# Optimization experiments

Hardware: AMD Instinct MI355X
Metric: run time of the kernel (lower is better)

Reference implementation:

```python
import jax, jax.numpy as jnp
import numpy as np

B, S, D, H, DH = 2, 2048, 1024, 16, 64

def setup_inputs() -> dict:
    key = jax.random.key(0)
    ks = jax.random.split(key, 9)
    sc = 0.02
    return {
        "x":  jax.random.normal(ks[0], (B, S, D), jnp.float32),
        "Wq": jax.random.normal(ks[1], (H, D, DH), jnp.float32) * sc,
        "bq": jax.random.normal(ks[2], (H, DH), jnp.float32) * sc,
        "Wk": jax.random.normal(ks[3], (H, D, DH), jnp.float32) * sc,
        "bk": jax.random.normal(ks[4], (H, DH), jnp.float32) * sc,
        "Wv": jax.random.normal(ks[5], (H, D, DH), jnp.float32) * sc,
        "bv": jax.random.normal(ks[6], (H, DH), jnp.float32) * sc,
        "Wo": jax.random.normal(ks[7], (D, D), jnp.float32) * sc,
        "bo": jax.random.normal(ks[8], (D,), jnp.float32) * sc,
    }

def reference(x, Wq, bq, Wk, bk, Wv, bv, Wo, bo):
    # Fused version of the per-head Python loop: all H heads batched.
    # q,k,v: [B,H,S,DH]
    q = jnp.einsum("bsi,hid->bhsd", x, Wq) + bq[None, :, None, :]
    k = jnp.einsum("bsi,hid->bhsd", x, Wk) + bk[None, :, None, :]
    v = jnp.einsum("bsi,hid->bhsd", x, Wv) + bv[None, :, None, :]
    scale = 1.0 / jnp.sqrt(jnp.asarray(DH, x.dtype))
    scores = jnp.einsum("bhsd,bhtd->bhst", q, k) * scale  # [B,H,S,S]
    attn = jax.nn.softmax(scores, axis=-1)
    o = jnp.einsum("bhst,bhtd->bhsd", attn, v)            # [B,H,S,DH]
    # torch.cat([head_0,...,head_{H-1}], dim=-1) -> [B,S,H*DH]
    o = jnp.transpose(o, (0, 2, 1, 3)).reshape(B, S, H * DH)
    # Dropout is identity in eval mode; final dense projection.
    return jnp.einsum("bsi,io->bso", o, Wo) + bo
```

## Files before the change

### kernel.cpp

```cpp
#include <hip/hip_runtime.h>
#include <hip/hip_bf16.h>

#define BB 2
#define SS 2048
#define DD 1024
#define HH 16
#define DHH 64

typedef __attribute__((ext_vector_type(8))) __bf16 bf16x8;
typedef __attribute__((ext_vector_type(4))) float f32x4;
typedef __attribute__((ext_vector_type(16))) float f32x16;
typedef __attribute__((ext_vector_type(4))) int i32x4;
typedef __attribute__((ext_vector_type(4))) unsigned int u32x4;

#define MFMA16 __builtin_amdgcn_mfma_f32_16x16x32_bf16
#define MFMA32 __builtin_amdgcn_mfma_f32_32x32x16_bf16

__device__ __forceinline__ unsigned short f2b(float f) {
  __hip_bfloat16 h = __float2bfloat16(f);
  unsigned short u;
  __builtin_memcpy(&u, &h, 2);
  return u;
}

__device__ __forceinline__ float exp2_fast(float x) {
  float r;
  asm("v_exp_f32 %0, %1" : "=v"(r) : "v"(x));
  return r;
}

__device__ __forceinline__ unsigned int cvtpk_bf16(float lo, float hi) {
  unsigned int r;
  asm("v_cvt_pk_bf16_f32 %0, %1, %2" : "=v"(r) : "v"(lo), "v"(hi));
  return r;
}

__device__ __forceinline__ void gl_lds16(const void* g, void* l) {
  __builtin_amdgcn_global_load_lds((const __attribute__((address_space(1))) void*)g,
                                   (__attribute__((address_space(3))) void*)l, 16, 0, 0);
}

__global__ __launch_bounds__(256) void k_cast(const float* __restrict__ in,
                                              unsigned short* __restrict__ out, int n4) {
  int i = blockIdx.x * blockDim.x + threadIdx.x;
  if (i >= n4) return;
  float4 v = ((const float4*)in)[i];
  ushort4 o;
  o.x = f2b(v.x); o.y = f2b(v.y); o.z = f2b(v.z); o.w = f2b(v.w);
  ((ushort4*)out)[i] = o;
}

__global__ __launch_bounds__(256) void k_tcast(const float* __restrict__ in,
                                               unsigned short* __restrict__ out, int R, int C) {
  __shared__ float t[32][33];
  size_t mb = (size_t)blockIdx.z * R * C;
  const float* im = in + mb;
  unsigned short* om = out + mb;
  int c0 = blockIdx.x * 32, r0 = blockIdx.y * 32;
  int tx = threadIdx.x & 31, ty = threadIdx.x >> 5;
#pragma unroll
  for (int rr = ty; rr < 32; rr += 8)
    t[rr][tx] = im[(size_t)(r0 + rr) * C + c0 + tx];
  __syncthreads();
#pragma unroll
  for (int rr = ty; rr < 32; rr += 8)
    om[(size_t)(c0 + rr) * R + r0 + tx] = f2b(t[tx][rr]);
}

__global__ __launch_bounds__(256) void k_tcast3(const float* __restrict__ Wq,
                                                const float* __restrict__ Wk,
                                                const float* __restrict__ Wv,
                                                unsigned short* __restrict__ out) {
  __shared__ float t[32][33];
  int z = blockIdx.z;
  const float* im = (z < 16 ? Wq : (z < 32 ? Wk : Wv)) + (size_t)(z & 15) * DD * DHH;
  unsigned short* om = out + (size_t)z * DD * DHH;
  int c0 = blockIdx.x * 32, r0 = blockIdx.y * 32;
  int tx = threadIdx.x & 31, ty = threadIdx.x >> 5;
#pragma unroll
  for (int rr = ty; rr < 32; rr += 8)
    t[rr][tx] = im[(size_t)(r0 + rr) * DHH + c0 + tx];
  __syncthreads();
#pragma unroll
  for (int rr = ty; rr < 32; rr += 8)
    om[(size_t)(c0 + rr) * DD + r0 + tx] = f2b(t[tx][rr]);
}

__global__ __launch_bounds__(256) void k_qkv(const unsigned short* __restrict__ A,
                                             const unsigned short* __restrict__ Wt,
                                             const float* __restrict__ bq,
                                             const float* __restrict__ bk,
                                             const float* __restrict__ bv,
                                             unsigned short* __restrict__ Qb,
                                             unsigned short* __restrict__ Kb,
                                             unsigned short* __restrict__ Vtb) {
  __shared__ __align__(16) unsigned short As[128 * 64];
  __shared__ __align__(16) unsigned short Bs[128 * 64];
  int tid = threadIdx.x;
  int w = tid >> 6, l = tid & 63, lr = l & 15, lg = l >> 4;
  int wr = w >> 1, wc = w & 1;
  int col0 = blockIdx.x * 128, row0 = blockIdx.y * 128;
  int sel = col0 >> 10;
  bool vsel = (sel == 2);
  const float* biasp = sel == 0 ? bq : (sel == 1 ? bk : bv);
  unsigned short* outp = sel == 0 ? Qb : Kb;
  float qscale = sel == 0 ? 0.18033688011112042f : 1.0f;

  int r8 = l >> 3, c8 = l & 7;
  const unsigned short* Ab = A + (size_t)(row0 + w * 32 + r8) * DD + c8 * 8;
  const unsigned short* Bb = Wt + (size_t)(col0 + w * 32 + r8) * DD + c8 * 8;

  f32x4 zero = {0.f, 0.f, 0.f, 0.f};
  f32x4 acc[4][4];
#pragma unroll
  for (int m = 0; m < 4; m++)
#pragma unroll
    for (int n = 0; n < 4; n++) acc[m][n] = zero;

  for (int k0 = 0; k0 < DD; k0 += 64) {
    __syncthreads();
#pragma unroll
    for (int c = 0; c < 4; c++) {
      gl_lds16(Ab + (size_t)c * 8 * DD + k0, (char*)As + (w * 32 + c * 8) * 128);
      gl_lds16(Bb + (size_t)c * 8 * DD + k0, (char*)Bs + (w * 32 + c * 8) * 128);
    }
    __syncthreads();
#pragma unroll
    for (int kk = 0; kk < 2; kk++) {
      bf16x8 af[4], bfr[4];
#pragma unroll
      for (int m = 0; m < 4; m++)
        af[m] = *(const bf16x8*)&As[(wr * 64 + m * 16 + lr) * 64 + kk * 32 + lg * 8];
#pragma unroll
      for (int n = 0; n < 4; n++)
        bfr[n] = *(const bf16x8*)&Bs[(wc * 64 + n * 16 + lr) * 64 + kk * 32 + lg * 8];
      if (!vsel) {
#pragma unroll
        for (int m = 0; m < 4; m++)
#pragma unroll
          for (int n = 0; n < 4; n++)
            acc[m][n] = MFMA16(af[m], bfr[n], acc[m][n], 0, 0, 0);
      } else {
#pragma unroll
        for (int m = 0; m < 4; m++)
#pragma unroll
          for (int n = 0; n < 4; n++)
            acc[m][n] = MFMA16(bfr[n], af[m], acc[m][n], 0, 0, 0);
      }
    }
  }

  if (!vsel) {
#pragma unroll
    for (int n = 0; n < 4; n++) {
      int c = col0 + wc * 64 + n * 16 + lr;
      int h = (c >> 6) & 15;
      int d = c & 63;
      float bias = biasp[h * DHH + d];
#pragma unroll
      for (int m = 0; m < 4; m++) {
#pragma unroll
        for (int j = 0; j < 4; j++) {
          int row = row0 + wr * 64 + m * 16 + lg * 4 + j;
          int b = row >> 11, s = row & 2047;
          outp[((size_t)(b * HH + h) * SS + s) * DHH + d] = f2b((acc[m][n][j] + bias) * qscale);
        }
      }
    }
  } else {
    int b = row0 >> 11, s0 = row0 & 2047;
#pragma unroll
    for (int n = 0; n < 4; n++) {
#pragma unroll
      for (int j = 0; j < 4; j++) {
        int dl = wc * 64 + n * 16 + lg * 4 + j;
        int hh = ((col0 & 1023) + dl) >> 6;
        int d = dl & 63;
        float bias = bv[hh * DHH + d];
#pragma unroll
        for (int m = 0; m < 4; m++) {
          int sl = wr * 64 + m * 16 + lr;
          Vtb[((size_t)(b * HH + hh) * DHH + d) * SS + s0 + sl] = f2b(acc[m][n][j] + bias);
        }
      }
    }
  }
}

__global__ __launch_bounds__(256) void k_proj(const unsigned short* __restrict__ A,
                                              const unsigned short* __restrict__ Wt,
                                              const float* __restrict__ bo,
                                              float* __restrict__ out) {
  __shared__ __align__(16) unsigned short As[128 * 64];
  __shared__ __align__(16) unsigned short Bs[128 * 64];
  int tid = threadIdx.x;
  int w = tid >> 6, l = tid & 63, lr = l & 15, lg = l >> 4;
  int wr = w >> 1, wc = w & 1;
  int col0 = blockIdx.x * 128, row0 = blockIdx.y * 128;

  int r8 = l >> 3, c8 = l & 7;
  const unsigned short* Ab = A + (size_t)(row0 + w * 32 + r8) * DD + c8 * 8;
  const unsigned short* Bb = Wt + (size_t)(col0 + w * 32 + r8) * DD + c8 * 8;

  f32x4 zero = {0.f, 0.f, 0.f, 0.f};
  f32x4 acc[4][4];
#pragma unroll
  for (int m = 0; m < 4; m++)
#pragma unroll
    for (int n = 0; n < 4; n++) acc[m][n] = zero;

  for (int k0 = 0; k0 < DD; k0 += 64) {
    __syncthreads();
#pragma unroll
    for (int c = 0; c < 4; c++) {
      gl_lds16(Ab + (size_t)c * 8 * DD + k0, (char*)As + (w * 32 + c * 8) * 128);
      gl_lds16(Bb + (size_t)c * 8 * DD + k0, (char*)Bs + (w * 32 + c * 8) * 128);
    }
    __syncthreads();
#pragma unroll
    for (int kk = 0; kk < 2; kk++) {
      bf16x8 af[4], bfr[4];
#pragma unroll
      for (int m = 0; m < 4; m++)
        af[m] = *(const bf16x8*)&As[(wr * 64 + m * 16 + lr) * 64 + kk * 32 + lg * 8];
#pragma unroll
      for (int n = 0; n < 4; n++)
        bfr[n] = *(const bf16x8*)&Bs[(wc * 64 + n * 16 + lr) * 64 + kk * 32 + lg * 8];
#pragma unroll
      for (int m = 0; m < 4; m++)
#pragma unroll
        for (int n = 0; n < 4; n++)
          acc[m][n] = MFMA16(af[m], bfr[n], acc[m][n], 0, 0, 0);
    }
  }

#pragma unroll
  for (int n = 0; n < 4; n++) {
    int c = col0 + wc * 64 + n * 16 + lr;
    float bias = bo[c];
#pragma unroll
    for (int m = 0; m < 4; m++) {
#pragma unroll
      for (int j = 0; j < 4; j++) {
        int row = row0 + wr * 64 + m * 16 + lg * 4 + j;
        out[(size_t)row * DD + c] = acc[m][n][j] + bias;
      }
    }
  }
}

#define QT 128
#define KVB 128
#define NTILE (SS / KVB)

__global__ __launch_bounds__(256, 2) void k_attn(const unsigned short* __restrict__ Q,
                                                 const unsigned short* __restrict__ K,
                                                 const unsigned short* __restrict__ Vt,
                                                 unsigned short* __restrict__ Ocat) {
  __shared__ __align__(16) char sm[81920];

  int tid = threadIdx.x;
  int w = tid >> 6, lane = tid & 63;
  int q32 = lane & 31, hi = lane >> 5;
  bool lo = (hi == 0);

  int n = blockIdx.x;
  int bh = ((n & 7) << 2) | ((n >> 3) & 3);
  int q0 = (n >> 5) * QT;
  int bi = bh >> 4, h = bh & 15;
  const unsigned short* Qm = Q + (size_t)bh * SS * DHH;
  const unsigned short* Km = K + (size_t)bh * SS * DHH;
  const unsigned short* Vm = Vt + (size_t)bh * DHH * SS;

  int l8r = lane >> 3, l8c = lane & 7;
  int cgK = l8c ^ l8r;
  int l16r = lane >> 4, l16c = lane & 15;

#pragma unroll
  for (int c = 0; c < 4; c++) {
    int base = w * 32 + c * 8;
    gl_lds16(Qm + (size_t)(q0 + base + l8r) * DHH + cgK * 8, sm + base * 128);
    gl_lds16(Km + (size_t)(base + l8r) * DHH + cgK * 8, sm + 16384 + base * 128);
  }
#pragma unroll
  for (int c = 0; c < 4; c++) {
    int based = w * 16 + c * 4;
    int cgV = l16c ^ (c * 4 + l16r);
    gl_lds16(Vm + (size_t)(based + l16r) * SS + cgV * 8, sm + 49152 + based * 256);
  }
  __syncthreads();

  bf16x8 qf[4];
  {
    int r = w * 32 + q32;
    const char* qb = sm + r * 128;
    int sw = (r & 7) << 4;
#pragma unroll
    for (int ks = 0; ks < 4; ks++)
      qf[ks] = *(const bf16x8*)(qb + ((ks * 32 + hi * 16) ^ sw));
  }

  f32x16 oacc0 = {}, oacc1 = {};
  float m_ = -1e30f, l_ = 0.f;
  const int sw3 = (q32 & 7) << 4;
  const int sw4 = (q32 & 15) << 4;

#define MKPA(PB, u) do { \
    unsigned int x0 = cvtpk_bf16(PB[8*(u)+0], PB[8*(u)+1]); \
    unsigned int x1 = cvtpk_bf16(PB[8*(u)+2], PB[8*(u)+3]); \
    unsigned int y0 = cvtpk_bf16(PB[8*(u)+4], PB[8*(u)+5]); \
    unsigned int y1 = cvtpk_bf16(PB[8*(u)+6], PB[8*(u)+7]); \
    unsigned int sx0 = (unsigned int)__shfl_xor((int)x0, 32); \
    unsigned int sx1 = (unsigned int)__shfl_xor((int)x1, 32); \
    unsigned int sy0 = (unsigned int)__shfl_xor((int)y0, 32); \
    unsigned int sy1 = (unsigned int)__shfl_xor((int)y1, 32); \
    pa[0] = lo ? x0 : sy0; pa[1] = lo ? x1 : sy1; \
    pa[2] = lo ? sx0 : y0; pa[3] = lo ? sx1 : y1; \
  } while (0)

#define PVSTEP(s) do { \
    bf16x8 pf = *(bf16x8*)&pa; \
    bf16x8 vf0 = *(const bf16x8*)(Vc + (q32) * 256 + (((s) * 32 + hi * 16) ^ sw4)); \
    bf16x8 vf1 = *(const bf16x8*)(Vc + (32 + q32) * 256 + (((s) * 32 + hi * 16) ^ sw4)); \
    oacc0 = MFMA32(vf0, pf, oacc0, 0, 0, 0); \
    oacc1 = MFMA32(vf1, pf, oacc1, 0, 0, 0); \
  } while (0)

  for (int t = 0; t < NTILE; t++) {
    const char* Kc = sm + 16384 + (t & 1) * 16384;
    const char* Vc = sm + 49152 + (t & 1) * 16384;

    if (t + 1 < NTILE) {
      int kv0 = (t + 1) * KVB;
      char* kd = sm + 16384 + ((t + 1) & 1) * 16384;
      char* vd = sm + 49152 + ((t + 1) & 1) * 16384;
#pragma unroll
      for (int c = 0; c < 4; c++) {
        int base = w * 32 + c * 8;
        gl_lds16(Km + (size_t)(kv0 + base + l8r) * DHH + cgK * 8, kd + base * 128);
      }
#pragma unroll
      for (int c = 0; c < 4; c++) {
        int based = w * 16 + c * 4;
        int cgV = l16c ^ (c * 4 + l16r);
        gl_lds16(Vm + (size_t)(based + l16r) * SS + kv0 + cgV * 8, vd + based * 256);
      }
    }

    f32x16 p0 = {}, p1 = {}, p2 = {}, p3 = {};
    __builtin_amdgcn_s_setprio(1);
#pragma unroll
    for (int ks = 0; ks < 4; ks++) {
      int co = (ks * 32 + hi * 16) ^ sw3;
      bf16x8 k0 = *(const bf16x8*)(Kc + (q32) * 128 + co);
      bf16x8 k1 = *(const bf16x8*)(Kc + (32 + q32) * 128 + co);
      bf16x8 k2 = *(const bf16x8*)(Kc + (64 + q32) * 128 + co);
      bf16x8 k3 = *(const bf16x8*)(Kc + (96 + q32) * 128 + co);
      p0 = MFMA32(k0, qf[ks], p0, 0, 0, 0);
      p1 = MFMA32(k1, qf[ks], p1, 0, 0, 0);
      p2 = MFMA32(k2, qf[ks], p2, 0, 0, 0);
      p3 = MFMA32(k3, qf[ks], p3, 0, 0, 0);
    }
    __builtin_amdgcn_s_setprio(0);

    float t16[16];
#pragma unroll
    for (int r = 0; r < 16; r++)
      t16[r] = fmaxf(fmaxf(p0[r], p1[r]), fmaxf(p2[r], p3[r]));
#pragma unroll
    for (int r = 0; r < 8; r++) t16[r] = fmaxf(t16[r], t16[r + 8]);
#pragma unroll
    for (int r = 0; r < 4; r++) t16[r] = fmaxf(t16[r], t16[r + 4]);
    float tmax = fmaxf(fmaxf(t16[0], t16[1]), fmaxf(t16[2], t16[3]));
    tmax = fmaxf(tmax, __shfl_xor(tmax, 32));

    if (__any(tmax > m_ + 8.0f)) {
      float nm = fmaxf(m_, tmax);
      float al = exp2_fast(m_ - nm);
      m_ = nm; l_ *= al;
#pragma unroll
      for (int r = 0; r < 16; r++) { oacc0[r] *= al; oacc1[r] *= al; }
    }

#pragma unroll
    for (int r = 0; r < 16; r++) p0[r] = exp2_fast(p0[r] - m_);
#pragma unroll
    for (int r = 0; r < 16; r++) p1[r] = exp2_fast(p1[r] - m_);
#pragma unroll
    for (int r = 0; r < 16; r++) p2[r] = exp2_fast(p2[r] - m_);
#pragma unroll
    for (int r = 0; r < 16; r++) p3[r] = exp2_fast(p3[r] - m_);
    float s16[16];
#pragma unroll
    for (int r = 0; r < 16; r++) s16[r] = (p0[r] + p1[r]) + (p2[r] + p3[r]);
#pragma unroll
    for (int r = 0; r < 8; r++) s16[r] += s16[r + 8];
#pragma unroll
    for (int r = 0; r < 4; r++) s16[r] += s16[r + 4];
    float ssum = (s16[0] + s16[1]) + (s16[2] + s16[3]);
    ssum += __shfl_xor(ssum, 32);
    l_ += ssum;

    __builtin_amdgcn_s_setprio(1);
    u32x4 pa;
    MKPA(p0, 0); PVSTEP(0);
    MKPA(p0, 1); PVSTEP(1);
    MKPA(p1, 0); PVSTEP(2);
    MKPA(p1, 1); PVSTEP(3);
    MKPA(p2, 0); PVSTEP(4);
    MKPA(p2, 1); PVSTEP(5);
    MKPA(p3, 0); PVSTEP(6);
    MKPA(p3, 1); PVSTEP(7);
    __builtin_amdgcn_s_setprio(0);

    __syncthreads();
  }

  float inv = 1.0f / l_;
  unsigned short* Os = (unsigned short*)sm;
  int rowq = w * 32 + q32;
#pragma unroll
  for (int r = 0; r < 16; r++) {
    int d = (r & 3) + 8 * (r >> 2) + 4 * hi;
    Os[rowq * 72 + d] = f2b(oacc0[r] * inv);
    Os[rowq * 72 + 32 + d] = f2b(oacc1[r] * inv);
  }
  __syncthreads();
#pragma unroll
  for (int i = 0; i < 4; i++) {
    int ci = tid + i * 256;
    int r = ci >> 3, c = ci & 7;
    i32x4 v = *(const i32x4*)(Os + r * 72 + c * 8);
    *(i32x4*)(Ocat + ((size_t)(bi * SS + q0 + r)) * DD + h * DHH + c * 8) = v;
  }
}

extern "C" void kernel_launch(void* const* d_in, const int* in_sizes, int n_in,
                              void* d_out, int out_size, void* d_ws, size_t ws_size,
                              hipStream_t stream) {
  const float* x  = (const float*)d_in[0];
  const float* Wq = (const float*)d_in[1];
  const float* bq = (const float*)d_in[2];
  const float* Wk = (const float*)d_in[3];
  const float* bk = (const float*)d_in[4];
  const float* Wv = (const float*)d_in[5];
  const float* bv = (const float*)d_in[6];
  const float* Wo = (const float*)d_in[7];
  const float* bo = (const float*)d_in[8];
  float* out = (float*)d_out;

  char* ws = (char*)d_ws;
  unsigned short* xb    = (unsigned short*)(ws);
  unsigned short* wqkvt = (unsigned short*)(ws + (size_t)(8u  << 20));
  unsigned short* wot   = (unsigned short*)(ws + (size_t)(14u << 20));
  unsigned short* Qb    = (unsigned short*)(ws + (size_t)(16u << 20));
  unsigned short* Kb    = (unsigned short*)(ws + (size_t)(24u << 20));
  unsigned short* Vt    = (unsigned short*)(ws + (size_t)(32u << 20));
  unsigned short* Ocat  = (unsigned short*)(ws + (size_t)(40u << 20));

  k_cast<<<(BB * SS * DD / 4 + 255) / 256, 256, 0, stream>>>(x, xb, BB * SS * DD / 4);
  k_tcast3<<<dim3(DHH / 32, DD / 32, 48), 256, 0, stream>>>(Wq, Wk, Wv, wqkvt);
  k_tcast<<<dim3(DD / 32, DD / 32, 1), 256, 0, stream>>>(Wo, wot, DD, DD);
  k_qkv<<<dim3(3 * DD / 128, BB * SS / 128), 256, 0, stream>>>(xb, wqkvt, bq, bk, bv, Qb, Kb, Vt);
  k_attn<<<dim3((SS / QT) * BB * HH), 256, 0, stream>>>(Qb, Kb, Vt, Ocat);
  k_proj<<<dim3(DD / 128, BB * SS / 128), 256, 0, stream>>>(Ocat, wot, bo, out);
}
```

Before: 141.1 us.

## Fuse prep casts, stage QKV epilogue via LDS, rewrite attention as single-wave register-streamed

Merges the three cast/transpose kernels into a single k_prep launch to cut launch overhead. The QKV GEMM epilogue now writes its tile to shared memory and stores 16-byte rows, replacing scattered 2-byte global writes for Q, K and transposed V. The attention kernel becomes one 64-lane wave per 32-query block. It loads K and V fragments straight from global memory into registers, double-buffering K across 64-key steps instead of using LDS tiles. This drops LDS traffic and barriers but relies on L2/cache hits for K/V reuse across blocks and has much less data sharing per block.

```diff
diff --git a/kernel.cpp b/kernel.cpp
--- a/kernel.cpp
+++ b/kernel.cpp
@@ -29,9 +29,9 @@
   return r;
 }
 
-__device__ __forceinline__ unsigned int cvtpk_bf16(float lo, float hi) {
+__device__ __forceinline__ unsigned int cvtpk_bf16(float lo_, float hi_) {
   unsigned int r;
-  asm("v_cvt_pk_bf16_f32 %0, %1, %2" : "=v"(r) : "v"(lo), "v"(hi));
+  asm("v_cvt_pk_bf16_f32 %0, %1, %2" : "=v"(r) : "v"(lo_), "v"(hi_));
   return r;
 }
 
@@ -40,23 +40,40 @@
                                    (__attribute__((address_space(3))) void*)l, 16, 0, 0);
 }
 
-__global__ __launch_bounds__(256) void k_cast(const float* __restrict__ in,
-                                              unsigned short* __restrict__ out, int n4) {
-  int i = blockIdx.x * blockDim.x + threadIdx.x;
-  if (i >= n4) return;
-  float4 v = ((const float4*)in)[i];
-  ushort4 o;
-  o.x = f2b(v.x); o.y = f2b(v.y); o.z = f2b(v.z); o.w = f2b(v.w);
-  ((ushort4*)out)[i] = o;
-}
-
-__global__ __launch_bounds__(256) void k_tcast(const float* __restrict__ in,
-                                               unsigned short* __restrict__ out, int R, int C) {
+__global__ __launch_bounds__(256) void k_prep(const float* __restrict__ x,
+                                              const float* __restrict__ Wq,
+                                              const float* __restrict__ Wk,
+                                              const float* __restrict__ Wv,
+                                              const float* __restrict__ Wo,
+                                              unsigned short* __restrict__ xb,
+                                              unsigned short* __restrict__ wqkvt,
+                                              unsigned short* __restrict__ wot) {
+  int blk = blockIdx.x;
+  if (blk < 4096) {
+    int i = blk * 256 + threadIdx.x;
+    float4 v = ((const float4*)x)[i];
+    ushort4 o;
+    o.x = f2b(v.x); o.y = f2b(v.y); o.z = f2b(v.z); o.w = f2b(v.w);
+    ((ushort4*)xb)[i] = o;
+    return;
+  }
   __shared__ float t[32][33];
-  size_t mb = (size_t)blockIdx.z * R * C;
-  const float* im = in + mb;
-  unsigned short* om = out + mb;
-  int c0 = blockIdx.x * 32, r0 = blockIdx.y * 32;
+  const float* im;
+  unsigned short* om;
+  int R, C, c0, r0;
+  if (blk < 7168) {
+    int bi2 = blk - 4096;
+    int z = bi2 >> 6, rem = bi2 & 63;
+    im = (z < 16 ? Wq : (z < 32 ? Wk : Wv)) + (size_t)(z & 15) * DD * DHH;
+    om = wqkvt + (size_t)z * DD * DHH;
+    R = DD; C = DHH;
+    c0 = (rem & 1) * 32; r0 = (rem >> 1) * 32;
+  } else {
+    int bi2 = blk - 7168;
+    im = Wo; om = wot;
+    R = DD; C = DD;
+    c0 = (bi2 & 31) * 32; r0 = (bi2 >> 5) * 32;
+  }
   int tx = threadIdx.x & 31, ty = threadIdx.x >> 5;
 #pragma unroll
   for (int rr = ty; rr < 32; rr += 8)
@@ -65,25 +82,6 @@
 #pragma unroll
   for (int rr = ty; rr < 32; rr += 8)
     om[(size_t)(c0 + rr) * R + r0 + tx] = f2b(t[tx][rr]);
-}
-
-__global__ __launch_bounds__(256) void k_tcast3(const float* __restrict__ Wq,
-                                                const float* __restrict__ Wk,
-                                                const float* __restrict__ Wv,
-                                                unsigned short* __restrict__ out) {
-  __shared__ float t[32][33];
-  int z = blockIdx.z;
-  const float* im = (z < 16 ? Wq : (z < 32 ? Wk : Wv)) + (size_t)(z & 15) * DD * DHH;
-  unsigned short* om = out + (size_t)z * DD * DHH;
-  int c0 = blockIdx.x * 32, r0 = blockIdx.y * 32;
-  int tx = threadIdx.x & 31, ty = threadIdx.x >> 5;
-#pragma unroll
-  for (int rr = ty; rr < 32; rr += 8)
-    t[rr][tx] = im[(size_t)(r0 + rr) * DHH + c0 + tx];
-  __syncthreads();
-#pragma unroll
-  for (int rr = ty; rr < 32; rr += 8)
-    om[(size_t)(c0 + rr) * DD + r0 + tx] = f2b(t[tx][rr]);
 }
 
 __global__ __launch_bounds__(256) void k_qkv(const unsigned short* __restrict__ A,
@@ -94,8 +92,9 @@
                                              unsigned short* __restrict__ Qb,
                                              unsigned short* __restrict__ Kb,
                                              unsigned short* __restrict__ Vtb) {
-  __shared__ __align__(16) unsigned short As[128 * 64];
-  __shared__ __align__(16) unsigned short Bs[128 * 64];
+  __shared__ __align__(16) unsigned short SMEM[128 * 136];
+  unsigned short* As = SMEM;
+  unsigned short* Bs = SMEM + 128 * 64;
   int tid = threadIdx.x;
   int w = tid >> 6, l = tid & 63, lr = l & 15, lg = l >> 4;
   int wr = w >> 1, wc = w & 1;
@@ -150,39 +149,59 @@
     }
   }
 
+  __syncthreads();
+  unsigned short* Ts = SMEM;
   if (!vsel) {
 #pragma unroll
     for (int n = 0; n < 4; n++) {
-      int c = col0 + wc * 64 + n * 16 + lr;
-      int h = (c >> 6) & 15;
-      int d = c & 63;
-      float bias = biasp[h * DHH + d];
+      int cl = wc * 64 + n * 16 + lr;
+      float bias = biasp[(col0 + cl) & 1023];
 #pragma unroll
       for (int m = 0; m < 4; m++) {
 #pragma unroll
         for (int j = 0; j < 4; j++) {
-          int row = row0 + wr * 64 + m * 16 + lg * 4 + j;
-          int b = row >> 11, s = row & 2047;
-          outp[((size_t)(b * HH + h) * SS + s) * DHH + d] = f2b((acc[m][n][j] + bias) * qscale);
+          int sl = wr * 64 + m * 16 + lg * 4 + j;
+          Ts[sl * 136 + cl] = f2b((acc[m][n][j] + bias) * qscale);
         }
       }
     }
+    __syncthreads();
+    int trow = tid >> 4, tc = tid & 15;
+#pragma unroll
+    for (int pass = 0; pass < 8; pass++) {
+      int sl = pass * 16 + trow;
+      int c0l = tc * 8;
+      i32x4 v = *(const i32x4*)&Ts[sl * 136 + c0l];
+      int c = col0 + c0l;
+      int hh = (c >> 6) & 15, d = c & 63;
+      int row = row0 + sl;
+      int b = row >> 11, s = row & 2047;
+      *(i32x4*)(outp + ((size_t)(b * HH + hh) * SS + s) * DHH + d) = v;
+    }
   } else {
-    int b = row0 >> 11, s0 = row0 & 2047;
 #pragma unroll
     for (int n = 0; n < 4; n++) {
 #pragma unroll
       for (int j = 0; j < 4; j++) {
-        int dl = wc * 64 + n * 16 + lg * 4 + j;
-        int hh = ((col0 & 1023) + dl) >> 6;
-        int d = dl & 63;
-        float bias = bv[hh * DHH + d];
+        int cl = wc * 64 + n * 16 + lg * 4 + j;
+        float bias = bv[((col0 & 1023) + cl) & 1023];
 #pragma unroll
         for (int m = 0; m < 4; m++) {
           int sl = wr * 64 + m * 16 + lr;
-          Vtb[((size_t)(b * HH + hh) * DHH + d) * SS + s0 + sl] = f2b(acc[m][n][j] + bias);
+          Ts[cl * 136 + sl] = f2b(acc[m][n][j] + bias);
         }
       }
+    }
+    __syncthreads();
+    int trow = tid >> 4, tc = tid & 15;
+    int b = row0 >> 11, s0 = row0 & 2047;
+#pragma unroll
+    for (int pass = 0; pass < 8; pass++) {
+      int cl = pass * 16 + trow;
+      int s8 = tc * 8;
+      i32x4 v = *(const i32x4*)&Ts[cl * 136 + s8];
+      int cg = (col0 & 1023) + cl;
+      *(i32x4*)(Vtb + (size_t)(b * 1024 + cg) * SS + s0 + s8) = v;
     }
   }
 }
@@ -249,61 +268,34 @@
   }
 }
 
-#define QT 128
-#define KVB 128
-#define NTILE (SS / KVB)
-
-__global__ __launch_bounds__(256, 2) void k_attn(const unsigned short* __restrict__ Q,
-                                                 const unsigned short* __restrict__ K,
-                                                 const unsigned short* __restrict__ Vt,
-                                                 unsigned short* __restrict__ Ocat) {
-  __shared__ __align__(16) char sm[81920];
-
-  int tid = threadIdx.x;
-  int w = tid >> 6, lane = tid & 63;
+__global__ __launch_bounds__(64, 2) void k_attn(const unsigned short* __restrict__ Q,
+                                                const unsigned short* __restrict__ K,
+                                                const unsigned short* __restrict__ Vt,
+                                                unsigned short* __restrict__ Ocat) {
+  __shared__ __align__(16) unsigned short Os[32 * 72];
+
+  int lane = threadIdx.x;
   int q32 = lane & 31, hi = lane >> 5;
   bool lo = (hi == 0);
 
   int n = blockIdx.x;
-  int bh = ((n & 7) << 2) | ((n >> 3) & 3);
-  int q0 = (n >> 5) * QT;
+  int bh = ((n & 7) << 2) | ((n >> 9) & 3);
+  int q0 = ((n >> 3) & 63) * 32;
   int bi = bh >> 4, h = bh & 15;
   const unsigned short* Qm = Q + (size_t)bh * SS * DHH;
-  const unsigned short* Km = K + (size_t)bh * SS * DHH;
-  const unsigned short* Vm = Vt + (size_t)bh * DHH * SS;
-
-  int l8r = lane >> 3, l8c = lane & 7;
-  int cgK = l8c ^ l8r;
-  int l16r = lane >> 4, l16c = lane & 15;
-
-#pragma unroll
-  for (int c = 0; c < 4; c++) {
-    int base = w * 32 + c * 8;
-    gl_lds16(Qm + (size_t)(q0 + base + l8r) * DHH + cgK * 8, sm + base * 128);
-    gl_lds16(Km + (size_t)(base + l8r) * DHH + cgK * 8, sm + 16384 + base * 128);
-  }
-#pragma unroll
-  for (int c = 0; c < 4; c++) {
-    int based = w * 16 + c * 4;
-    int cgV = l16c ^ (c * 4 + l16r);
-    gl_lds16(Vm + (size_t)(based + l16r) * SS + cgV * 8, sm + 49152 + based * 256);
-  }
-  __syncthreads();
+  const unsigned short* kp = K + (size_t)bh * SS * DHH + q32 * DHH + hi * 8;
+  const unsigned short* vp = Vt + (size_t)bh * DHH * SS + (size_t)q32 * SS + hi * 8;
 
   bf16x8 qf[4];
   {
-    int r = w * 32 + q32;
-    const char* qb = sm + r * 128;
-    int sw = (r & 7) << 4;
+    const unsigned short* qrow = Qm + (size_t)(q0 + q32) * DHH + hi * 8;
 #pragma unroll
     for (int ks = 0; ks < 4; ks++)
-      qf[ks] = *(const bf16x8*)(qb + ((ks * 32 + hi * 16) ^ sw));
+      qf[ks] = *(const bf16x8*)(qrow + ks * 16);
   }
 
   f32x16 oacc0 = {}, oacc1 = {};
   float m_ = -1e30f, l_ = 0.f;
-  const int sw3 = (q32 & 7) << 4;
-  const int sw4 = (q32 & 15) << 4;
 
 #define MKPA(PB, u) do { \
     unsigned int x0 = cvtpk_bf16(PB[8*(u)+0], PB[8*(u)+1]); \
@@ -320,119 +312,100 @@
 
 #define PVSTEP(s) do { \
     bf16x8 pf = *(bf16x8*)&pa; \
-    bf16x8 vf0 = *(const bf16x8*)(Vc + (q32) * 256 + (((s) * 32 + hi * 16) ^ sw4)); \
-    bf16x8 vf1 = *(const bf16x8*)(Vc + (32 + q32) * 256 + (((s) * 32 + hi * 16) ^ sw4)); \
-    oacc0 = MFMA32(vf0, pf, oacc0, 0, 0, 0); \
-    oacc1 = MFMA32(vf1, pf, oacc1, 0, 0, 0); \
+    oacc0 = MFMA32(vf[(s)], pf, oacc0, 0, 0, 0); \
+    oacc1 = MFMA32(vf[4 + (s)], pf, oacc1, 0, 0, 0); \
   } while (0)
 
-  for (int t = 0; t < NTILE; t++) {
-    const char* Kc = sm + 16384 + (t & 1) * 16384;
-    const char* Vc = sm + 49152 + (t & 1) * 16384;
-
-    if (t + 1 < NTILE) {
-      int kv0 = (t + 1) * KVB;
-      char* kd = sm + 16384 + ((t + 1) & 1) * 16384;
-      char* vd = sm + 49152 + ((t + 1) & 1) * 16384;
-#pragma unroll
-      for (int c = 0; c < 4; c++) {
-        int base = w * 32 + c * 8;
-        gl_lds16(Km + (size_t)(kv0 + base + l8r) * DHH + cgK * 8, kd + base * 128);
-      }
-#pragma unroll
-      for (int c = 0; c < 4; c++) {
-        int based = w * 16 + c * 4;
-        int cgV = l16c ^ (c * 4 + l16r);
-        gl_lds16(Vm + (size_t)(based + l16r) * SS + kv0 + cgV * 8, vd + based * 256);
-      }
-    }
-
-    f32x16 p0 = {}, p1 = {}, p2 = {}, p3 = {};
-    __builtin_amdgcn_s_setprio(1);
-#pragma unroll
-    for (int ks = 0; ks < 4; ks++) {
-      int co = (ks * 32 + hi * 16) ^ sw3;
-      bf16x8 k0 = *(const bf16x8*)(Kc + (q32) * 128 + co);
-      bf16x8 k1 = *(const bf16x8*)(Kc + (32 + q32) * 128 + co);
-      bf16x8 k2 = *(const bf16x8*)(Kc + (64 + q32) * 128 + co);
-      bf16x8 k3 = *(const bf16x8*)(Kc + (96 + q32) * 128 + co);
-      p0 = MFMA32(k0, qf[ks], p0, 0, 0, 0);
-      p1 = MFMA32(k1, qf[ks], p1, 0, 0, 0);
-      p2 = MFMA32(k2, qf[ks], p2, 0, 0, 0);
-      p3 = MFMA32(k3, qf[ks], p3, 0, 0, 0);
-    }
-    __builtin_amdgcn_s_setprio(0);
-
-    float t16[16];
-#pragma unroll
-    for (int r = 0; r < 16; r++)
-      t16[r] = fmaxf(fmaxf(p0[r], p1[r]), fmaxf(p2[r], p3[r]));
-#pragma unroll
-    for (int r = 0; r < 8; r++) t16[r] = fmaxf(t16[r], t16[r + 8]);
-#pragma unroll
-    for (int r = 0; r < 4; r++) t16[r] = fmaxf(t16[r], t16[r + 4]);
-    float tmax = fmaxf(fmaxf(t16[0], t16[1]), fmaxf(t16[2], t16[3]));
-    tmax = fmaxf(tmax, __shfl_xor(tmax, 32));
-
-    if (__any(tmax > m_ + 8.0f)) {
-      float nm = fmaxf(m_, tmax);
-      float al = exp2_fast(m_ - nm);
-      m_ = nm; l_ *= al;
-#pragma unroll
-      for (int r = 0; r < 16; r++) { oacc0[r] *= al; oacc1[r] *= al; }
-    }
-
-#pragma unroll
-    for (int r = 0; r < 16; r++) p0[r] = exp2_fast(p0[r] - m_);
-#pragma unroll
-    for (int r = 0; r < 16; r++) p1[r] = exp2_fast(p1[r] - m_);
-#pragma unroll
-    for (int r = 0; r < 16; r++) p2[r] = exp2_fast(p2[r] - m_);
-#pragma unroll
-    for (int r = 0; r < 16; r++) p3[r] = exp2_fast(p3[r] - m_);
-    float s16[16];
-#pragma unroll
-    for (int r = 0; r < 16; r++) s16[r] = (p0[r] + p1[r]) + (p2[r] + p3[r]);
-#pragma unroll
-    for (int r = 0; r < 8; r++) s16[r] += s16[r + 8];
-#pragma unroll
-    for (int r = 0; r < 4; r++) s16[r] += s16[r + 4];
-    float ssum = (s16[0] + s16[1]) + (s16[2] + s16[3]);
-    ssum += __shfl_xor(ssum, 32);
-    l_ += ssum;
-
-    __builtin_amdgcn_s_setprio(1);
-    u32x4 pa;
-    MKPA(p0, 0); PVSTEP(0);
-    MKPA(p0, 1); PVSTEP(1);
-    MKPA(p1, 0); PVSTEP(2);
-    MKPA(p1, 1); PVSTEP(3);
-    MKPA(p2, 0); PVSTEP(4);
-    MKPA(p2, 1); PVSTEP(5);
-    MKPA(p3, 0); PVSTEP(6);
-    MKPA(p3, 1); PVSTEP(7);
-    __builtin_amdgcn_s_setprio(0);
-
-    __syncthreads();
-  }
-
+#define ATTN_BODY(CUR, NXT, T) do { \
+    int kv0 = (T) * 64; \
+    bf16x8 vf[8]; \
+    _Pragma("unroll") \
+    for (int db = 0; db < 2; db++) \
+      _Pragma("unroll") \
+      for (int s = 0; s < 4; s++) \
+        vf[db * 4 + s] = *(const bf16x8*)(vp + (size_t)db * 32 * SS + kv0 + s * 16); \
+    f32x16 p0 = {}, p1 = {}; \
+    _Pragma("unroll") \
+    for (int ks = 0; ks < 4; ks++) { \
+      p0 = MFMA32(CUR[ks], qf[ks], p0, 0, 0, 0); \
+      p1 = MFMA32(CUR[4 + ks], qf[ks], p1, 0, 0, 0); \
+    } \
+    if ((T) + 1 < 32) { \
+      const unsigned short* kn = kp + (size_t)((T) + 1) * 64 * DHH; \
+      _Pragma("unroll") \
+      for (int b2 = 0; b2 < 2; b2++) \
+        _Pragma("unroll") \
+        for (int ks = 0; ks < 4; ks++) \
+          NXT[b2 * 4 + ks] = *(const bf16x8*)(kn + b2 * 32 * DHH + ks * 16); \
+    } \
+    float t8[8]; \
+    _Pragma("unroll") \
+    for (int r = 0; r < 8; r++) \
+      t8[r] = fmaxf(fmaxf(p0[r], p0[r + 8]), fmaxf(p1[r], p1[r + 8])); \
+    _Pragma("unroll") \
+    for (int r = 0; r < 4; r++) t8[r] = fmaxf(t8[r], t8[r + 4]); \
+    float tmax = fmaxf(fmaxf(t8[0], t8[1]), fmaxf(t8[2], t8[3])); \
+    tmax = fmaxf(tmax, __shfl_xor(tmax, 32)); \
+    if (__any(tmax > m_ + 8.0f)) { \
+      float nm = fmaxf(m_, tmax); \
+      float al = exp2_fast(m_ - nm); \
+      m_ = nm; l_ *= al; \
+      _Pragma("unroll") \
+      for (int r = 0; r < 16; r++) { oacc0[r] *= al; oacc1[r] *= al; } \
+    } \
+    _Pragma("unroll") \
+    for (int r = 0; r < 16; r++) p0[r] = exp2_fast(p0[r] - m_); \
+    _Pragma("unroll") \
+    for (int r = 0; r < 16; r++) p1[r] = exp2_fast(p1[r] - m_); \
+    float s8[8]; \
+    _Pragma("unroll") \
+    for (int r = 0; r < 8; r++) s8[r] = (p0[r] + p0[r + 8]) + (p1[r] + p1[r + 8]); \
+    _Pragma("unroll") \
+    for (int r = 0; r < 4; r++) s8[r] += s8[r + 4]; \
+    l_ += ((s8[0] + s8[1]) + (s8[2] + s8[3])); \
+    u32x4 pa; \
+    MKPA(p0, 0); PVSTEP(0); \
+    MKPA(p0, 1); PVSTEP(1); \
+    MKPA(p1, 0); PVSTEP(2); \
+    MKPA(p1, 1); PVSTEP(3); \
+  } while (0)
+
+  bf16x8 kfA[8], kfB[8];
+#pragma unroll
+  for (int b2 = 0; b2 < 2; b2++)
+#pragma unroll
+    for (int ks = 0; ks < 4; ks++)
+      kfA[b2 * 4 + ks] = *(const bf16x8*)(kp + b2 * 32 * DHH + ks * 16);
+
+  for (int t = 0; t < 32; t += 2) {
+    ATTN_BODY(kfA, kfB, t);
+    ATTN_BODY(kfB, kfA, t + 1);
+  }
+
+  l_ += __shfl_xor(l_, 32);
   float inv = 1.0f / l_;
-  unsigned short* Os = (unsigned short*)sm;
-  int rowq = w * 32 + q32;
-#pragma unroll
-  for (int r = 0; r < 16; r++) {
-    int d = (r & 3) + 8 * (r >> 2) + 4 * hi;
-    Os[rowq * 72 + d] = f2b(oacc0[r] * inv);
-    Os[rowq * 72 + 32 + d] = f2b(oacc1[r] * inv);
+#pragma unroll
+  for (int g = 0; g < 4; g++) {
+    unsigned int w0 = cvtpk_bf16(oacc0[g * 4 + 0] * inv, oacc0[g * 4 + 1] * inv);
+    unsigned int w1 = cvtpk_bf16(oacc0[g * 4 + 2] * inv, oacc0[g * 4 + 3] * inv);
+    *(unsigned int*)&Os[q32 * 72 + g * 8 + 4 * hi] = w0;
+    *(unsigned int*)&Os[q32 * 72 + g * 8 + 4 * hi + 2] = w1;
+    unsigned int w2 = cvtpk_bf16(oacc1[g * 4 + 0] * inv, oacc1[g * 4 + 1] * inv);
+    unsigned int w3 = cvtpk_bf16(oacc1[g * 4 + 2] * inv, oacc1[g * 4 + 3] * inv);
+    *(unsigned int*)&Os[q32 * 72 + 32 + g * 8 + 4 * hi] = w2;
+    *(unsigned int*)&Os[q32 * 72 + 32 + g * 8 + 4 * hi + 2] = w3;
   }
   __syncthreads();
 #pragma unroll
-  for (int i = 0; i < 4; i++) {
-    int ci = tid + i * 256;
-    int r = ci >> 3, c = ci & 7;
-    i32x4 v = *(const i32x4*)(Os + r * 72 + c * 8);
-    *(i32x4*)(Ocat + ((size_t)(bi * SS + q0 + r)) * DD + h * DHH + c * 8) = v;
-  }
+  for (int pass = 0; pass < 4; pass++) {
+    int row = pass * 8 + (lane >> 3);
+    int c8 = (lane & 7) * 8;
+    i32x4 v = *(const i32x4*)&Os[row * 72 + c8];
+    *(i32x4*)(Ocat + ((size_t)(bi * SS + q0 + row)) * DD + h * DHH + c8) = v;
+  }
+#undef MKPA
+#undef PVSTEP
+#undef ATTN_BODY
 }
 
 extern "C" void kernel_launch(void* const* d_in, const int* in_sizes, int n_in,
@@ -458,10 +431,8 @@
   unsigned short* Vt    = (unsigned short*)(ws + (size_t)(32u << 20));
   unsigned short* Ocat  = (unsigned short*)(ws + (size_t)(40u << 20));
 
-  k_cast<<<(BB * SS * DD / 4 + 255) / 256, 256, 0, stream>>>(x, xb, BB * SS * DD / 4);
-  k_tcast3<<<dim3(DHH / 32, DD / 32, 48), 256, 0, stream>>>(Wq, Wk, Wv, wqkvt);
-  k_tcast<<<dim3(DD / 32, DD / 32, 1), 256, 0, stream>>>(Wo, wot, DD, DD);
+  k_prep<<<8192, 256, 0, stream>>>(x, Wq, Wk, Wv, Wo, xb, wqkvt, wot);
   k_qkv<<<dim3(3 * DD / 128, BB * SS / 128), 256, 0, stream>>>(xb, wqkvt, bq, bk, bv, Qb, Kb, Vt);
-  k_attn<<<dim3((SS / QT) * BB * HH), 256, 0, stream>>>(Qb, Kb, Vt, Ocat);
+  k_attn<<<dim3(2048), 64, 0, stream>>>(Qb, Kb, Vt, Ocat);
   k_proj<<<dim3(DD / 128, BB * SS / 128), 256, 0, stream>>>(Ocat, wot, bo, out);
 }
```

New measurement: 200.6 us. +42.2%, slower.
